# Kernel tuning notes

Hardware: AMD Instinct MI355X
Metric: run time of the kernel (lower is better)

## Reference

```python
import jax, jax.numpy as jnp
import numpy as np

N_NODES = 100000
N_EDGES = 1600000
N_GRAPHS = 512


def gcn_conv(x, row, col, W, b):
    # x: [N, Cin], row/col: [E] (self-loops already appended)
    n = x.shape[0]
    h = x @ W                                        # [N, Cout]
    deg = jax.ops.segment_sum(jnp.ones_like(col, dtype=x.dtype), col, num_segments=n)
    dinv = jnp.where(deg > 0, deg ** -0.5, 0.0)
    norm = dinv[row] * dinv[col]                     # [E]
    msg = norm[:, None] * h[row]                     # [E, Cout]
    out = jax.ops.segment_sum(msg, col, num_segments=n)
    return out + b


def setup_inputs() -> dict:
    key = jax.random.key(0)
    ks = jax.random.split(key, 10)
    x = jax.random.normal(ks[0], (N_NODES, 128), dtype=jnp.float32)
    edge_index = jax.random.randint(ks[1], (2, N_EDGES), 0, N_NODES, dtype=jnp.int64)
    batch = jnp.sort(jax.random.randint(ks[2], (N_NODES,), 0, N_GRAPHS, dtype=jnp.int64))
    def lin_w(k, fan_in, fan_out):
        bound = 1.0 / np.sqrt(fan_in)
        return jax.random.uniform(k, (fan_in, fan_out), jnp.float32, -bound, bound)
    # GCN layers (bias zero-initialized per reset_parameters)
    W1 = lin_w(ks[3], 128, 128); b1 = jnp.zeros((128,), jnp.float32)
    W2 = lin_w(ks[4], 128, 128); b2 = jnp.zeros((128,), jnp.float32)
    # MLP layers (Linear with bias)
    Wm1 = lin_w(ks[5], 128, 64)
    bm1 = jax.random.uniform(ks[6], (64,), jnp.float32, -1/np.sqrt(128), 1/np.sqrt(128))
    Wm2 = lin_w(ks[7], 64, 1)
    bm2 = jax.random.uniform(ks[8], (1,), jnp.float32, -1/np.sqrt(64), 1/np.sqrt(64))
    return {"x": x, "edge_index": edge_index, "batch": batch,
            "W1": W1, "b1": b1, "W2": W2, "b2": b2,
            "Wm1": Wm1, "bm1": bm1, "Wm2": Wm2, "bm2": bm2}


def reference(x, edge_index, batch, W1, b1, W2, b2, Wm1, bm1, Wm2, bm2):
    n = x.shape[0]
    loops = jnp.arange(n, dtype=edge_index.dtype)
    row = jnp.concatenate([edge_index[0], loops])
    col = jnp.concatenate([edge_index[1], loops])
    # GCN: conv -> relu -> conv
    h = gcn_conv(x, row, col, W1, b1)
    h = jax.nn.relu(h)
    h = gcn_conv(h, row, col, W2, b2)
    # scatter-mean pooling over graphs
    sums = jax.ops.segment_sum(h, batch, num_segments=N_GRAPHS)      # [G, C]
    counts = jax.ops.segment_sum(jnp.ones((n,), h.dtype), batch, num_segments=N_GRAPHS)
    g = sums / jnp.maximum(counts, 1.0)[:, None]
    # MLP: linear -> relu -> linear
    g = jax.nn.relu(g @ Wm1 + bm1)
    out = g @ Wm2 + bm2
    return out
```

## Files before the change

### kernel.cpp

```cpp
#include <hip/hip_runtime.h>
#include <math.h>

#define C_DIM 128
#define POOL_CHUNK 64
#define BKT_SHIFT 7
#define MAX_B 1024
#define CB 256
#define FB_CAP 8192
typedef unsigned short ushort_t;
typedef __attribute__((ext_vector_type(8))) short short8;
typedef __attribute__((ext_vector_type(4))) float f32x4;

static inline int ceil_div(int a, int b) { return (a + b - 1) / b; }

__device__ inline ushort_t f2bf(float f) {
    union { float f; unsigned u; } v; v.f = f;
    unsigned r = v.u + 0x7FFFu + ((v.u >> 16) & 1u);
    return (ushort_t)(r >> 16);
}
__device__ inline float bf2f(unsigned s) {
    union { unsigned u; float f; } v; v.u = s << 16; return v.f;
}
__device__ inline float bf_lo(unsigned u) {
    union { unsigned v; float f; } c; c.v = u << 16; return c.f;
}
__device__ inline float bf_hi(unsigned u) {
    union { unsigned v; float f; } c; c.v = u & 0xFFFF0000u; return c.f;
}


__global__ __launch_bounds__(256) void k_bcount(
    const int* __restrict__ col, int E, int chunk, int B,
    int* __restrict__ counts) {
    __shared__ int hist[MAX_B];
    int t = threadIdx.x;
    for (int i = t; i < B; i += 256) hist[i] = 0;
    __syncthreads();
    int s = blockIdx.x * chunk;
    int e = s + chunk; if (e > E) e = E;
    for (int i = s + 4 * t; i < e; i += 1024) {
        int4 c = *(const int4*)(col + i);
        atomicAdd(&hist[c.x >> BKT_SHIFT], 1);
        atomicAdd(&hist[c.y >> BKT_SHIFT], 1);
        atomicAdd(&hist[c.z >> BKT_SHIFT], 1);
        atomicAdd(&hist[c.w >> BKT_SHIFT], 1);
    }
    __syncthreads();
    for (int i = t; i < B; i += 256)
        counts[(size_t)i * CB + blockIdx.x] = hist[i];
}

__global__ __launch_bounds__(256) void k_bscan(
    int* __restrict__ counts, int* __restrict__ btot) {
    __shared__ int sd[256];
    int b = blockIdx.x, t = threadIdx.x;
    int v = counts[(size_t)b * CB + t];
    sd[t] = v;
    __syncthreads();
    for (int off = 1; off < 256; off <<= 1) {
        int x = (t >= off) ? sd[t - off] : 0;
        __syncthreads();
        sd[t] += x;
        __syncthreads();
    }
    counts[(size_t)b * CB + t] = sd[t] - v;
    if (t == 255) btot[b] = sd[255];
}

__global__ __launch_bounds__(256) void k_btotscan(
    const int* __restrict__ btot, int* __restrict__ bbase, int B, int E,
    int* __restrict__ offs, int N) {
    __shared__ int sd[256];
    __shared__ int carry_s;
    int t = threadIdx.x;
    if (t == 0) carry_s = 0;
    __syncthreads();
    int nc = (B + 255) / 256;
    for (int c = 0; c < nc; ++c) {
        int idx = c * 256 + t;
        int v = (idx < B) ? btot[idx] : 0;
        sd[t] = v;
        __syncthreads();
        for (int off = 1; off < 256; off <<= 1) {
            int x = (t >= off) ? sd[t - off] : 0;
            __syncthreads();
            sd[t] += x;
            __syncthreads();
        }
        int pre = sd[t] - v + carry_s;
        if (idx < B) bbase[idx] = pre;
        __syncthreads();
        if (t == 0) carry_s += sd[255];
        __syncthreads();
    }
    if (t == 0) { bbase[B] = E; offs[N] = E; }
}

__global__ __launch_bounds__(256) void k_bscatter(
    const int* __restrict__ row, const int* __restrict__ col, int E, int chunk,
    int B, const int* __restrict__ counts, const int* __restrict__ bbase,
    int* __restrict__ epk) {
    __shared__ int cur[MAX_B];
    int t = threadIdx.x, blk = blockIdx.x;
    for (int i = t; i < B; i += 256)
        cur[i] = bbase[i] + counts[(size_t)i * CB + blk];
    __syncthreads();
    int s = blk * chunk;
    int e = s + chunk; if (e > E) e = E;
    for (int i = s + 4 * t; i < e; i += 1024) {
        int4 c = *(const int4*)(col + i);
        int4 r = *(const int4*)(row + i);
        int s0 = atomicAdd(&cur[c.x >> BKT_SHIFT], 1); epk[s0] = (r.x << 7) | (c.x & 127);
        int s1 = atomicAdd(&cur[c.y >> BKT_SHIFT], 1); epk[s1] = (r.y << 7) | (c.y & 127);
        int s2 = atomicAdd(&cur[c.z >> BKT_SHIFT], 1); epk[s2] = (r.z << 7) | (c.z & 127);
        int s3 = atomicAdd(&cur[c.w >> BKT_SHIFT], 1); epk[s3] = (r.w << 7) | (c.w & 127);
    }
}

__global__ __launch_bounds__(256) void k_bfinal(
    const int* __restrict__ epk, const int* __restrict__ bbase, int N,
    int* __restrict__ offs, float* __restrict__ dinv, int* __restrict__ csr) {
    __shared__ int sh[FB_CAP];
    __shared__ int cnt[128];
    __shared__ int pre[128];
    __shared__ int cur[128];
    int bkt = blockIdx.x, t = threadIdx.x;
    int s = bbase[bkt], e = bbase[bkt + 1];
    int m = e - s;
    int base = bkt << BKT_SHIFT;
    int nn = N - base; if (nn > 128) nn = 128;
    bool fits = (m <= FB_CAP);
    if (t < 128) cnt[t] = 0;
    __syncthreads();
    if (fits) {
        for (int i = t; i < m; i += 256) {
            int u = epk[s + i];
            sh[i] = u;
            atomicAdd(&cnt[u & 127], 1);
        }
    } else {
        for (int i = s + t; i < e; i += 256)
            atomicAdd(&cnt[epk[i] & 127], 1);
    }
    __syncthreads();
    if (t < 128) pre[t] = cnt[t];
    __syncthreads();
    for (int off = 1; off < 128; off <<= 1) {
        int x = (t >= off && t < 128) ? pre[t - off] : 0;
        __syncthreads();
        if (t < 128) pre[t] += x;
        __syncthreads();
    }
    if (t < 128) {
        int ex = pre[t] - cnt[t];
        cur[t] = ex;
        if (t < nn) {
            offs[base + t] = s + ex;
            dinv[base + t] = 1.0f / sqrtf((float)cnt[t] + 1.0f);
        }
    }
    __syncthreads();
    if (fits) {
        for (int i = t; i < m; i += 256) {
            int u = sh[i];
            int slot = atomicAdd(&cur[u & 127], 1);
            csr[s + slot] = u >> 7;
        }
    } else {
        for (int i = s + t; i < e; i += 256) {
            int u = epk[i];
            int slot = atomicAdd(&cur[u & 127], 1);
            csr[s + slot] = u >> 7;
        }
    }
}

__global__ __launch_bounds__(256) void k_wfrag2(
    const float* __restrict__ W1, const float* __restrict__ W2,
    uint4* __restrict__ wf1, uint4* __restrict__ wf2) {
    const float* W = blockIdx.x ? W2 : W1;
    uint4* wf = blockIdx.x ? wf2 : wf1;
    int t = threadIdx.x;
    for (int f = t; f < 2048; f += 256) {
        int lane = f & 63, kkn = f >> 6;
        int kk = kkn & 3, nt = kkn >> 2;
        int n = lane & 15, quad = lane >> 4;
        union { ushort_t h[8]; uint4 v; } u;
#pragma unroll
        for (int j = 0; j < 8; ++j)
            u.h[j] = f2bf(W[(size_t)(kk * 32 + quad * 8 + j) * C_DIM + nt * 16 + n]);
        wf[f] = u.v;
    }
}

template <int ABF16>
__global__ __launch_bounds__(256) void k_matmul_mfma(
    const float* __restrict__ Af, const ushort_t* __restrict__ Abf,
    const uint4* __restrict__ wfrag, const float* __restrict__ dinv,
    ushort_t* __restrict__ Cb, int N) {
    __shared__ uint4 wfs[2048];
    __shared__ __align__(16) ushort_t eb[64 * 136];
    int t = threadIdx.x;
    int wv = t >> 6, lane = t & 63;
    int n = lane & 15, quad = lane >> 4;
    int row0 = blockIdx.x * 128;

    for (int i = t; i < 2048; i += 256) wfs[i] = wfrag[i];

    int rA[2];
#pragma unroll
    for (int tl = 0; tl < 2; ++tl) {
        int r = row0 + wv * 32 + tl * 16 + n;
        rA[tl] = r < N ? r : N - 1;
    }

    f32x4 acc[2][8];
#pragma unroll
    for (int tl = 0; tl < 2; ++tl)
#pragma unroll
        for (int i = 0; i < 8; ++i) acc[tl][i] = (f32x4){0.f, 0.f, 0.f, 0.f};

    __syncthreads();

#pragma unroll
    for (int kk = 0; kk < 4; ++kk) {
        short8 a[2];
#pragma unroll
        for (int tl = 0; tl < 2; ++tl) {
            if (ABF16) {
                uint4 u = *(const uint4*)(Abf + (size_t)rA[tl] * C_DIM + kk * 32 + quad * 8);
                union { uint4 v; short8 s; } c; c.v = u;
                a[tl] = c.s;
            } else {
                const float4* ap = (const float4*)(Af + (size_t)rA[tl] * C_DIM + kk * 32 + quad * 8);
                float4 f0 = ap[0], f1 = ap[1];
                union { ushort_t h[8]; short8 s; } c;
                c.h[0] = f2bf(f0.x); c.h[1] = f2bf(f0.y); c.h[2] = f2bf(f0.z); c.h[3] = f2bf(f0.w);
                c.h[4] = f2bf(f1.x); c.h[5] = f2bf(f1.y); c.h[6] = f2bf(f1.z); c.h[7] = f2bf(f1.w);
                a[tl] = c.s;
            }
        }
#pragma unroll
        for (int nt = 0; nt < 8; ++nt) {
            uint4 bu = wfs[(nt * 4 + kk) * 64 + lane];
            union { uint4 v; short8 s; } c; c.v = bu;
            acc[0][nt] = __builtin_amdgcn_mfma_f32_16x16x32_bf16(a[0], c.s, acc[0][nt], 0, 0, 0);
            acc[1][nt] = __builtin_amdgcn_mfma_f32_16x16x32_bf16(a[1], c.s, acc[1][nt], 0, 0, 0);
        }
    }

#pragma unroll
    for (int pass = 0; pass < 2; ++pass) {
        __syncthreads();
#pragma unroll
        for (int reg = 0; reg < 4; ++reg) {
            int lr = quad * 4 + reg;
            int grow = row0 + wv * 32 + pass * 16 + lr;
            float sc = dinv[grow < N ? grow : N - 1];
#pragma unroll
            for (int nt = 0; nt < 8; ++nt)
                eb[(wv * 16 + lr) * 136 + nt * 16 + n] = f2bf(acc[pass][nt][reg] * sc);
        }
        __syncthreads();
        for (int idx = t; idx < 16 * 64; idx += 256) {
            int r = idx >> 4, c8 = idx & 15;
            int grow = row0 + (r >> 4) * 32 + pass * 16 + (r & 15);
            if (grow < N)
                *(uint4*)(Cb + (size_t)grow * C_DIM + c8 * 8) =
                    *(const uint4*)&eb[r * 136 + c8 * 8];
        }
    }
}

template <int RELU>
__global__ __launch_bounds__(256) void k_aggregate(
    const ushort_t* __restrict__ hs, const int* __restrict__ offs,
    const int* __restrict__ csr, const float* __restrict__ dinv,
    const float* __restrict__ bias, uint4* __restrict__ outV, int N) {
    int node = (blockIdx.x << 2) + (threadIdx.x >> 6);
    if (node >= N) return;
    int t = threadIdx.x & 63;
    int q = t >> 4;
    int fs = t & 15;
    int s = offs[node], e = offs[node + 1];

    float2 ac[4];
    {
        uint4 u = *(const uint4*)(hs + (size_t)node * C_DIM + fs * 8);
        if (q == 0) {
            ac[0] = make_float2(bf_lo(u.x), bf_hi(u.x));
            ac[1] = make_float2(bf_lo(u.y), bf_hi(u.y));
            ac[2] = make_float2(bf_lo(u.z), bf_hi(u.z));
            ac[3] = make_float2(bf_lo(u.w), bf_hi(u.w));
        } else {
#pragma unroll
            for (int i = 0; i < 4; ++i) ac[i] = make_float2(0.f, 0.f);
        }
    }

    int j = s;
    int head = (s + 3) & ~3; if (head > e) head = e;
    if (j < head) {
        if (j + q < head) {
            uint4 u = *(const uint4*)(hs + (size_t)csr[j + q] * C_DIM + fs * 8);
            ac[0].x += bf_lo(u.x); ac[0].y += bf_hi(u.x);
            ac[1].x += bf_lo(u.y); ac[1].y += bf_hi(u.y);
            ac[2].x += bf_lo(u.z); ac[2].y += bf_hi(u.z);
            ac[3].x += bf_lo(u.w); ac[3].y += bf_hi(u.w);
        }
        j = head;
    }
    for (; j + 16 <= e; j += 16) {
        int4 rv = *(const int4*)(csr + j + 4 * q);
        uint4 u0 = *(const uint4*)(hs + (size_t)rv.x * C_DIM + fs * 8);
        uint4 u1 = *(const uint4*)(hs + (size_t)rv.y * C_DIM + fs * 8);
        uint4 u2 = *(const uint4*)(hs + (size_t)rv.z * C_DIM + fs * 8);
        uint4 u3 = *(const uint4*)(hs + (size_t)rv.w * C_DIM + fs * 8);
        ac[0].x += bf_lo(u0.x); ac[0].y += bf_hi(u0.x);
        ac[1].x += bf_lo(u0.y); ac[1].y += bf_hi(u0.y);
        ac[2].x += bf_lo(u0.z); ac[2].y += bf_hi(u0.z);
        ac[3].x += bf_lo(u0.w); ac[3].y += bf_hi(u0.w);
        ac[0].x += bf_lo(u1.x); ac[0].y += bf_hi(u1.x);
        ac[1].x += bf_lo(u1.y); ac[1].y += bf_hi(u1.y);
        ac[2].x += bf_lo(u1.z); ac[2].y += bf_hi(u1.z);
        ac[3].x += bf_lo(u1.w); ac[3].y += bf_hi(u1.w);
        ac[0].x += bf_lo(u2.x); ac[0].y += bf_hi(u2.x);
        ac[1].x += bf_lo(u2.y); ac[1].y += bf_hi(u2.y);
        ac[2].x += bf_lo(u2.z); ac[2].y += bf_hi(u2.z);
        ac[3].x += bf_lo(u2.w); ac[3].y += bf_hi(u2.w);
        ac[0].x += bf_lo(u3.x); ac[0].y += bf_hi(u3.x);
        ac[1].x += bf_lo(u3.y); ac[1].y += bf_hi(u3.y);
        ac[2].x += bf_lo(u3.z); ac[2].y += bf_hi(u3.z);
        ac[3].x += bf_lo(u3.w); ac[3].y += bf_hi(u3.w);
    }
    for (; j + 4 <= e; j += 4) {
        uint4 u = *(const uint4*)(hs + (size_t)csr[j + q] * C_DIM + fs * 8);
        ac[0].x += bf_lo(u.x); ac[0].y += bf_hi(u.x);
        ac[1].x += bf_lo(u.y); ac[1].y += bf_hi(u.y);
        ac[2].x += bf_lo(u.z); ac[2].y += bf_hi(u.z);
        ac[3].x += bf_lo(u.w); ac[3].y += bf_hi(u.w);
    }
    if (j + q < e) {
        uint4 u = *(const uint4*)(hs + (size_t)csr[j + q] * C_DIM + fs * 8);
        ac[0].x += bf_lo(u.x); ac[0].y += bf_hi(u.x);
        ac[1].x += bf_lo(u.y); ac[1].y += bf_hi(u.y);
        ac[2].x += bf_lo(u.z); ac[2].y += bf_hi(u.z);
        ac[3].x += bf_lo(u.w); ac[3].y += bf_hi(u.w);
    }

#pragma unroll
    for (int i = 0; i < 4; ++i) {
        ac[i].x += __shfl_xor(ac[i].x, 16);
        ac[i].y += __shfl_xor(ac[i].y, 16);
        ac[i].x += __shfl_xor(ac[i].x, 32);
        ac[i].y += __shfl_xor(ac[i].y, 32);
    }

    if (q == 0) {
        float dn = dinv[node];
        float4 b0 = *(const float4*)(bias + fs * 8);
        float4 b1 = *(const float4*)(bias + fs * 8 + 4);
        float o[8];
        o[0] = dn * ac[0].x + b0.x; o[1] = dn * ac[0].y + b0.y;
        o[2] = dn * ac[1].x + b0.z; o[3] = dn * ac[1].y + b0.w;
        o[4] = dn * ac[2].x + b1.x; o[5] = dn * ac[2].y + b1.y;
        o[6] = dn * ac[3].x + b1.z; o[7] = dn * ac[3].y + b1.w;
        if (RELU) {
#pragma unroll
            for (int i = 0; i < 8; ++i) o[i] = fmaxf(o[i], 0.f);
        }
        uint4 pk;
        pk.x = (unsigned)f2bf(o[0]) | ((unsigned)f2bf(o[1]) << 16);
        pk.y = (unsigned)f2bf(o[2]) | ((unsigned)f2bf(o[3]) << 16);
        pk.z = (unsigned)f2bf(o[4]) | ((unsigned)f2bf(o[5]) << 16);
        pk.w = (unsigned)f2bf(o[6]) | ((unsigned)f2bf(o[7]) << 16);
        outV[(size_t)node * 16 + fs] = pk;
    }
}

__global__ __launch_bounds__(128) void k_pool_sum(
    const ushort_t* __restrict__ h, const int* __restrict__ batch, int n,
    float* __restrict__ sums) {
    int r0 = blockIdx.x * POOL_CHUNK;
    int r1 = r0 + POOL_CHUNK; if (r1 > n) r1 = n;
    if (r0 >= n) return;
    int t = threadIdx.x;
    int c = t & 63, rr = t >> 6;
    float2 acc = make_float2(0.f, 0.f);
    int g = batch[r0];
    int i = r0;
    while (i < r1) {
        if (i + 8 <= r1 && batch[i + 7] == g) {
#pragma unroll
            for (int b = 0; b < 4; ++b) {
                unsigned u = *(const unsigned*)(h + (size_t)(i + rr + 2 * b) * C_DIM + c * 2);
                acc.x += bf_lo(u); acc.y += bf_hi(u);
            }
            i += 8;
        } else {
            int bi = batch[i];
            if (bi != g) {
                atomicAdd(&sums[(size_t)g * C_DIM + c * 2], acc.x);
                atomicAdd(&sums[(size_t)g * C_DIM + c * 2 + 1], acc.y);
                acc = make_float2(0.f, 0.f); g = bi;
            }
            if (rr == 0) {
                unsigned u = *(const unsigned*)(h + (size_t)i * C_DIM + c * 2);
                acc.x += bf_lo(u); acc.y += bf_hi(u);
            }
            ++i;
        }
    }
    atomicAdd(&sums[(size_t)g * C_DIM + c * 2], acc.x);
    atomicAdd(&sums[(size_t)g * C_DIM + c * 2 + 1], acc.y);
}

__global__ __launch_bounds__(128) void k_mlp(
    const float* __restrict__ sums, const int* __restrict__ batch, int n,
    const float* __restrict__ Wm1, const float* __restrict__ bm1,
    const float* __restrict__ Wm2, const float* __restrict__ bm2,
    float* __restrict__ out) {
    int g = blockIdx.x;
    int t = threadIdx.x;
    int lo = 0, hi = n;
    while (lo < hi) { int m = (lo + hi) >> 1; if (batch[m] < g) lo = m + 1; else hi = m; }
    int start = lo;
    lo = start; hi = n;
    while (lo < hi) { int m = (lo + hi) >> 1; if (batch[m] < g + 1) lo = m + 1; else hi = m; }
    float cnt = (float)(lo - start);

    float mean = sums[(size_t)g * C_DIM + t] / fmaxf(cnt, 1.0f);

    __shared__ float m_s[128];
    __shared__ float hid[64];
    m_s[t] = mean;
    __syncthreads();
    if (t < 64) {
        float a = bm1[t];
#pragma unroll 4
        for (int k = 0; k < 128; ++k) a += m_s[k] * Wm1[k * 64 + t];
        hid[t] = fmaxf(a, 0.f) * Wm2[t];
    }
    __syncthreads();
    if (t < 64) {
        float v = hid[t];
        for (int off = 32; off > 0; off >>= 1) v += __shfl_down(v, off);
        if (t == 0) out[g] = v + bm2[0];
    }
}

extern "C" void kernel_launch(void* const* d_in, const int* in_sizes, int n_in,
                              void* d_out, int out_size, void* d_ws, size_t ws_size,
                              hipStream_t stream) {
    const float* x     = (const float*)d_in[0];
    const int*   eidx  = (const int*)d_in[1];
    const int*   batch = (const int*)d_in[2];
    const float* W1    = (const float*)d_in[3];
    const float* b1    = (const float*)d_in[4];
    const float* W2    = (const float*)d_in[5];
    const float* b2    = (const float*)d_in[6];
    const float* Wm1   = (const float*)d_in[7];
    const float* bm1   = (const float*)d_in[8];
    const float* Wm2   = (const float*)d_in[9];
    const float* bm2   = (const float*)d_in[10];

    const int N = in_sizes[2];
    const int E = in_sizes[1] / 2;
    const int G = out_size;
    const int B = (N + 127) >> BKT_SHIFT;

    char* p = (char*)d_ws;
    auto carve = [&](size_t bytes) {
        char* q = p;
        p += (bytes + 255) & ~(size_t)255;
        return q;
    };
    ushort_t* bufT   = (ushort_t*)carve((size_t)N * C_DIM * sizeof(ushort_t));
    ushort_t* bufA   = (ushort_t*)carve((size_t)N * C_DIM * sizeof(ushort_t));
    float*    dinv   = (float*)   carve((size_t)N * sizeof(float));
    int*      offs   = (int*)     carve((size_t)(N + 1) * sizeof(int));
    int*      csr    = (int*)     carve((size_t)E * sizeof(int));
    int*      counts = (int*)     carve((size_t)B * CB * sizeof(int));
    int*      btot   = (int*)     carve((size_t)B * sizeof(int));
    int*      bbase  = (int*)     carve((size_t)(B + 1) * sizeof(int));
    float*    gsums  = (float*)   carve((size_t)G * C_DIM * sizeof(float));
    uint4*    wf1    = (uint4*)   carve(2048 * sizeof(uint4));
    uint4*    wf2    = (uint4*)   carve(2048 * sizeof(uint4));
    int*      epk    = (int*)bufT;

    const int* erow = eidx;
    const int* ecol = eidx + E;
    const int chunk = (ceil_div(E, CB) + 3) & ~3;

    hipMemsetAsync(gsums, 0, (size_t)G * C_DIM * sizeof(float), stream);

    k_bcount<<<CB, 256, 0, stream>>>(ecol, E, chunk, B, counts);
    k_bscan<<<B, 256, 0, stream>>>(counts, btot);
    k_btotscan<<<1, 256, 0, stream>>>(btot, bbase, B, E, offs, N);
    k_bscatter<<<CB, 256, 0, stream>>>(erow, ecol, E, chunk, B, counts, bbase, epk);
    k_bfinal<<<B, 256, 0, stream>>>(epk, bbase, N, offs, dinv, csr);

    k_wfrag2<<<2, 256, 0, stream>>>(W1, W2, wf1, wf2);

    k_matmul_mfma<0><<<ceil_div(N, 128), 256, 0, stream>>>(x, nullptr, wf1, dinv, bufT, N);
    k_aggregate<1><<<ceil_div(N, 4), 256, 0, stream>>>(bufT, offs, csr, dinv, b1,
                                                       (uint4*)bufA, N);
    k_matmul_mfma<1><<<ceil_div(N, 128), 256, 0, stream>>>(nullptr, bufA, wf2, dinv, bufT, N);
    k_aggregate<0><<<ceil_div(N, 4), 256, 0, stream>>>(bufT, offs, csr, dinv, b2,
                                                       (uint4*)bufA, N);
    k_pool_sum<<<ceil_div(N, POOL_CHUNK), 128, 0, stream>>>(bufA, batch, N, gsums);
    k_mlp<<<G, 128, 0, stream>>>(gsums, batch, N, Wm1, bm1, Wm2, bm2, (float*)d_out);
}
```

Before: 341.7 us.

## Fold weight prep and memset into bcount, replace bucket scan with atomic cursor

Weight fragment conversion and the gsums zeroing move into extra blocks of k_bcount. The single-block total scan kernel is dropped: each bucket now claims its base offset through an atomicAdd on a global cursor, so buckets are no longer laid out in order, and offsets become int2 start/end pairs. The aggregate kernel drops its alignment head and loads csr indices as scalars instead of int4. The aim is to remove three launches and a serial scan, at the cost of a nondeterministic CSR layout and a possibly less coalesced edge order.

```diff
diff --git a/kernel.cpp b/kernel.cpp
--- a/kernel.cpp
+++ b/kernel.cpp
@@ -27,16 +27,43 @@
 __device__ inline float bf_hi(unsigned u) {
     union { unsigned v; float f; } c; c.v = u & 0xFFFF0000u; return c.f;
 }
+__device__ inline void accum8(uint4 u, float acc[8]) {
+    acc[0] += bf_lo(u.x); acc[1] += bf_hi(u.x);
+    acc[2] += bf_lo(u.y); acc[3] += bf_hi(u.y);
+    acc[4] += bf_lo(u.z); acc[5] += bf_hi(u.z);
+    acc[6] += bf_lo(u.w); acc[7] += bf_hi(u.w);
+}
 
 
 __global__ __launch_bounds__(256) void k_bcount(
     const int* __restrict__ col, int E, int chunk, int B,
-    int* __restrict__ counts) {
+    int* __restrict__ counts,
+    const float* __restrict__ W1, const float* __restrict__ W2,
+    uint4* __restrict__ wf1, uint4* __restrict__ wf2,
+    float* __restrict__ gsums, int GC, int* __restrict__ cursor) {
+    int t = threadIdx.x, blk = blockIdx.x;
+    if (blk >= CB) {
+        const float* W = (blk == CB) ? W1 : W2;
+        uint4* wf = (blk == CB) ? wf1 : wf2;
+        for (int f = t; f < 2048; f += 256) {
+            int lane = f & 63, kkn = f >> 6;
+            int kk = kkn & 3, nt = kkn >> 2;
+            int n = lane & 15, quad = lane >> 4;
+            union { ushort_t h[8]; uint4 v; } u;
+#pragma unroll
+            for (int j = 0; j < 8; ++j)
+                u.h[j] = f2bf(W[(size_t)(kk * 32 + quad * 8 + j) * C_DIM + nt * 16 + n]);
+            wf[f] = u.v;
+        }
+        return;
+    }
+    for (int i = blk * 256 + t; i < GC; i += CB * 256) gsums[i] = 0.f;
+    if (blk == 0 && t == 0) *cursor = 0;
+
     __shared__ int hist[MAX_B];
-    int t = threadIdx.x;
     for (int i = t; i < B; i += 256) hist[i] = 0;
     __syncthreads();
-    int s = blockIdx.x * chunk;
+    int s = blk * chunk;
     int e = s + chunk; if (e > E) e = E;
     for (int i = s + 4 * t; i < e; i += 1024) {
         int4 c = *(const int4*)(col + i);
@@ -47,11 +74,12 @@
     }
     __syncthreads();
     for (int i = t; i < B; i += 256)
-        counts[(size_t)i * CB + blockIdx.x] = hist[i];
+        counts[(size_t)i * CB + blk] = hist[i];
 }
 
 __global__ __launch_bounds__(256) void k_bscan(
-    int* __restrict__ counts, int* __restrict__ btot) {
+    int* __restrict__ counts, int* __restrict__ bbase, int* __restrict__ btot,
+    int* __restrict__ cursor) {
     __shared__ int sd[256];
     int b = blockIdx.x, t = threadIdx.x;
     int v = counts[(size_t)b * CB + t];
@@ -64,36 +92,10 @@
         __syncthreads();
     }
     counts[(size_t)b * CB + t] = sd[t] - v;
-    if (t == 255) btot[b] = sd[255];
-}
-
-__global__ __launch_bounds__(256) void k_btotscan(
-    const int* __restrict__ btot, int* __restrict__ bbase, int B, int E,
-    int* __restrict__ offs, int N) {
-    __shared__ int sd[256];
-    __shared__ int carry_s;
-    int t = threadIdx.x;
-    if (t == 0) carry_s = 0;
-    __syncthreads();
-    int nc = (B + 255) / 256;
-    for (int c = 0; c < nc; ++c) {
-        int idx = c * 256 + t;
-        int v = (idx < B) ? btot[idx] : 0;
-        sd[t] = v;
-        __syncthreads();
-        for (int off = 1; off < 256; off <<= 1) {
-            int x = (t >= off) ? sd[t - off] : 0;
-            __syncthreads();
-            sd[t] += x;
-            __syncthreads();
-        }
-        int pre = sd[t] - v + carry_s;
-        if (idx < B) bbase[idx] = pre;
-        __syncthreads();
-        if (t == 0) carry_s += sd[255];
-        __syncthreads();
-    }
-    if (t == 0) { bbase[B] = E; offs[N] = E; }
+    if (t == 255) {
+        btot[b] = sd[255];
+        bbase[b] = atomicAdd(cursor, sd[255]);
+    }
 }
 
 __global__ __launch_bounds__(256) void k_bscatter(
@@ -118,15 +120,17 @@
 }
 
 __global__ __launch_bounds__(256) void k_bfinal(
-    const int* __restrict__ epk, const int* __restrict__ bbase, int N,
-    int* __restrict__ offs, float* __restrict__ dinv, int* __restrict__ csr) {
+    const int* __restrict__ epk, const int* __restrict__ bbase,
+    const int* __restrict__ btot, int N,
+    int2* __restrict__ offs2, float* __restrict__ dinv, int* __restrict__ csr) {
     __shared__ int sh[FB_CAP];
     __shared__ int cnt[128];
     __shared__ int pre[128];
     __shared__ int cur[128];
     int bkt = blockIdx.x, t = threadIdx.x;
-    int s = bbase[bkt], e = bbase[bkt + 1];
-    int m = e - s;
+    int s = bbase[bkt];
+    int m = btot[bkt];
+    int e = s + m;
     int base = bkt << BKT_SHIFT;
     int nn = N - base; if (nn > 128) nn = 128;
     bool fits = (m <= FB_CAP);
@@ -155,7 +159,7 @@
         int ex = pre[t] - cnt[t];
         cur[t] = ex;
         if (t < nn) {
-            offs[base + t] = s + ex;
+            offs2[base + t] = make_int2(s + ex, s + ex + cnt[t]);
             dinv[base + t] = 1.0f / sqrtf((float)cnt[t] + 1.0f);
         }
     }
@@ -172,24 +176,6 @@
             int slot = atomicAdd(&cur[u & 127], 1);
             csr[s + slot] = u >> 7;
         }
-    }
-}
-
-__global__ __launch_bounds__(256) void k_wfrag2(
-    const float* __restrict__ W1, const float* __restrict__ W2,
-    uint4* __restrict__ wf1, uint4* __restrict__ wf2) {
-    const float* W = blockIdx.x ? W2 : W1;
-    uint4* wf = blockIdx.x ? wf2 : wf1;
-    int t = threadIdx.x;
-    for (int f = t; f < 2048; f += 256) {
-        int lane = f & 63, kkn = f >> 6;
-        int kk = kkn & 3, nt = kkn >> 2;
-        int n = lane & 15, quad = lane >> 4;
-        union { ushort_t h[8]; uint4 v; } u;
-#pragma unroll
-        for (int j = 0; j < 8; ++j)
-            u.h[j] = f2bf(W[(size_t)(kk * 32 + quad * 8 + j) * C_DIM + nt * 16 + n]);
-        wf[f] = u.v;
     }
 }
 
@@ -274,7 +260,7 @@
 
 template <int RELU>
 __global__ __launch_bounds__(256) void k_aggregate(
-    const ushort_t* __restrict__ hs, const int* __restrict__ offs,
+    const ushort_t* __restrict__ hs, const int2* __restrict__ offs2,
     const int* __restrict__ csr, const float* __restrict__ dinv,
     const float* __restrict__ bias, uint4* __restrict__ outV, int N) {
     int node = (blockIdx.x << 2) + (threadIdx.x >> 6);
@@ -282,78 +268,48 @@
     int t = threadIdx.x & 63;
     int q = t >> 4;
     int fs = t & 15;
-    int s = offs[node], e = offs[node + 1];
-
-    float2 ac[4];
+    int2 se = offs2[node];
+    int s = se.x, e = se.y;
+
+    float acc[8];
     {
         uint4 u = *(const uint4*)(hs + (size_t)node * C_DIM + fs * 8);
-        if (q == 0) {
-            ac[0] = make_float2(bf_lo(u.x), bf_hi(u.x));
-            ac[1] = make_float2(bf_lo(u.y), bf_hi(u.y));
-            ac[2] = make_float2(bf_lo(u.z), bf_hi(u.z));
-            ac[3] = make_float2(bf_lo(u.w), bf_hi(u.w));
-        } else {
-#pragma unroll
-            for (int i = 0; i < 4; ++i) ac[i] = make_float2(0.f, 0.f);
-        }
+        float v[8];
+        v[0] = bf_lo(u.x); v[1] = bf_hi(u.x);
+        v[2] = bf_lo(u.y); v[3] = bf_hi(u.y);
+        v[4] = bf_lo(u.z); v[5] = bf_hi(u.z);
+        v[6] = bf_lo(u.w); v[7] = bf_hi(u.w);
+#pragma unroll
+        for (int i = 0; i < 8; ++i) acc[i] = (q == 0) ? v[i] : 0.f;
     }
 
     int j = s;
-    int head = (s + 3) & ~3; if (head > e) head = e;
-    if (j < head) {
-        if (j + q < head) {
-            uint4 u = *(const uint4*)(hs + (size_t)csr[j + q] * C_DIM + fs * 8);
-            ac[0].x += bf_lo(u.x); ac[0].y += bf_hi(u.x);
-            ac[1].x += bf_lo(u.y); ac[1].y += bf_hi(u.y);
-            ac[2].x += bf_lo(u.z); ac[2].y += bf_hi(u.z);
-            ac[3].x += bf_lo(u.w); ac[3].y += bf_hi(u.w);
-        }
-        j = head;
-    }
     for (; j + 16 <= e; j += 16) {
-        int4 rv = *(const int4*)(csr + j + 4 * q);
-        uint4 u0 = *(const uint4*)(hs + (size_t)rv.x * C_DIM + fs * 8);
-        uint4 u1 = *(const uint4*)(hs + (size_t)rv.y * C_DIM + fs * 8);
-        uint4 u2 = *(const uint4*)(hs + (size_t)rv.z * C_DIM + fs * 8);
-        uint4 u3 = *(const uint4*)(hs + (size_t)rv.w * C_DIM + fs * 8);
-        ac[0].x += bf_lo(u0.x); ac[0].y += bf_hi(u0.x);
-        ac[1].x += bf_lo(u0.y); ac[1].y += bf_hi(u0.y);
-        ac[2].x += bf_lo(u0.z); ac[2].y += bf_hi(u0.z);
-        ac[3].x += bf_lo(u0.w); ac[3].y += bf_hi(u0.w);
-        ac[0].x += bf_lo(u1.x); ac[0].y += bf_hi(u1.x);
-        ac[1].x += bf_lo(u1.y); ac[1].y += bf_hi(u1.y);
-        ac[2].x += bf_lo(u1.z); ac[2].y += bf_hi(u1.z);
-        ac[3].x += bf_lo(u1.w); ac[3].y += bf_hi(u1.w);
-        ac[0].x += bf_lo(u2.x); ac[0].y += bf_hi(u2.x);
-        ac[1].x += bf_lo(u2.y); ac[1].y += bf_hi(u2.y);
-        ac[2].x += bf_lo(u2.z); ac[2].y += bf_hi(u2.z);
-        ac[3].x += bf_lo(u2.w); ac[3].y += bf_hi(u2.w);
-        ac[0].x += bf_lo(u3.x); ac[0].y += bf_hi(u3.x);
-        ac[1].x += bf_lo(u3.y); ac[1].y += bf_hi(u3.y);
-        ac[2].x += bf_lo(u3.z); ac[2].y += bf_hi(u3.z);
-        ac[3].x += bf_lo(u3.w); ac[3].y += bf_hi(u3.w);
+        int r[4];
+#pragma unroll
+        for (int b = 0; b < 4; ++b) r[b] = csr[j + b * 4 + q];
+        uint4 u[4];
+#pragma unroll
+        for (int b = 0; b < 4; ++b)
+            u[b] = *(const uint4*)(hs + (size_t)r[b] * C_DIM + fs * 8);
+#pragma unroll
+        for (int b = 0; b < 4; ++b) accum8(u[b], acc);
     }
     for (; j + 4 <= e; j += 4) {
-        uint4 u = *(const uint4*)(hs + (size_t)csr[j + q] * C_DIM + fs * 8);
-        ac[0].x += bf_lo(u.x); ac[0].y += bf_hi(u.x);
-        ac[1].x += bf_lo(u.y); ac[1].y += bf_hi(u.y);
-        ac[2].x += bf_lo(u.z); ac[2].y += bf_hi(u.z);
-        ac[3].x += bf_lo(u.w); ac[3].y += bf_hi(u.w);
+        int r = csr[j + q];
+        uint4 u = *(const uint4*)(hs + (size_t)r * C_DIM + fs * 8);
+        accum8(u, acc);
     }
     if (j + q < e) {
-        uint4 u = *(const uint4*)(hs + (size_t)csr[j + q] * C_DIM + fs * 8);
-        ac[0].x += bf_lo(u.x); ac[0].y += bf_hi(u.x);
-        ac[1].x += bf_lo(u.y); ac[1].y += bf_hi(u.y);
-        ac[2].x += bf_lo(u.z); ac[2].y += bf_hi(u.z);
-        ac[3].x += bf_lo(u.w); ac[3].y += bf_hi(u.w);
-    }
-
-#pragma unroll
-    for (int i = 0; i < 4; ++i) {
-        ac[i].x += __shfl_xor(ac[i].x, 16);
-        ac[i].y += __shfl_xor(ac[i].y, 16);
-        ac[i].x += __shfl_xor(ac[i].x, 32);
-        ac[i].y += __shfl_xor(ac[i].y, 32);
+        int r = csr[j + q];
+        uint4 u = *(const uint4*)(hs + (size_t)r * C_DIM + fs * 8);
+        accum8(u, acc);
+    }
+
+#pragma unroll
+    for (int i = 0; i < 8; ++i) {
+        acc[i] += __shfl_xor(acc[i], 16);
+        acc[i] += __shfl_xor(acc[i], 32);
     }
 
     if (q == 0) {
@@ -361,10 +317,10 @@
         float4 b0 = *(const float4*)(bias + fs * 8);
         float4 b1 = *(const float4*)(bias + fs * 8 + 4);
         float o[8];
-        o[0] = dn * ac[0].x + b0.x; o[1] = dn * ac[0].y + b0.y;
-        o[2] = dn * ac[1].x + b0.z; o[3] = dn * ac[1].y + b0.w;
-        o[4] = dn * ac[2].x + b1.x; o[5] = dn * ac[2].y + b1.y;
-        o[6] = dn * ac[3].x + b1.z; o[7] = dn * ac[3].y + b1.w;
+        o[0] = dn * acc[0] + b0.x; o[1] = dn * acc[1] + b0.y;
+        o[2] = dn * acc[2] + b0.z; o[3] = dn * acc[3] + b0.w;
+        o[4] = dn * acc[4] + b1.x; o[5] = dn * acc[5] + b1.y;
+        o[6] = dn * acc[6] + b1.z; o[7] = dn * acc[7] + b1.w;
         if (RELU) {
 #pragma unroll
             for (int i = 0; i < 8; ++i) o[i] = fmaxf(o[i], 0.f);
@@ -478,35 +434,32 @@
     ushort_t* bufT   = (ushort_t*)carve((size_t)N * C_DIM * sizeof(ushort_t));
     ushort_t* bufA   = (ushort_t*)carve((size_t)N * C_DIM * sizeof(ushort_t));
     float*    dinv   = (float*)   carve((size_t)N * sizeof(float));
-    int*      offs   = (int*)     carve((size_t)(N + 1) * sizeof(int));
+    int2*     offs2  = (int2*)    carve((size_t)N * sizeof(int2));
     int*      csr    = (int*)     carve((size_t)E * sizeof(int));
     int*      counts = (int*)     carve((size_t)B * CB * sizeof(int));
     int*      btot   = (int*)     carve((size_t)B * sizeof(int));
-    int*      bbase  = (int*)     carve((size_t)(B + 1) * sizeof(int));
+    int*      bbase  = (int*)     carve((size_t)B * sizeof(int));
     float*    gsums  = (float*)   carve((size_t)G * C_DIM * sizeof(float));
     uint4*    wf1    = (uint4*)   carve(2048 * sizeof(uint4));
     uint4*    wf2    = (uint4*)   carve(2048 * sizeof(uint4));
+    int*      cursor = (int*)     carve(sizeof(int));
     int*      epk    = (int*)bufT;
 
     const int* erow = eidx;
     const int* ecol = eidx + E;
     const int chunk = (ceil_div(E, CB) + 3) & ~3;
 
-    hipMemsetAsync(gsums, 0, (size_t)G * C_DIM * sizeof(float), stream);
-
-    k_bcount<<<CB, 256, 0, stream>>>(ecol, E, chunk, B, counts);
-    k_bscan<<<B, 256, 0, stream>>>(counts, btot);
-    k_btotscan<<<1, 256, 0, stream>>>(btot, bbase, B, E, offs, N);
+    k_bcount<<<CB + 2, 256, 0, stream>>>(ecol, E, chunk, B, counts,
+                                         W1, W2, wf1, wf2, gsums, G * C_DIM, cursor);
+    k_bscan<<<B, 256, 0, stream>>>(counts, bbase, btot, cursor);
     k_bscatter<<<CB, 256, 0, stream>>>(erow, ecol, E, chunk, B, counts, bbase, epk);
-    k_bfinal<<<B, 256, 0, stream>>>(epk, bbase, N, offs, dinv, csr);
-
-    k_wfrag2<<<2, 256, 0, stream>>>(W1, W2, wf1, wf2);
+    k_bfinal<<<B, 256, 0, stream>>>(epk, bbase, btot, N, offs2, dinv, csr);
 
     k_matmul_mfma<0><<<ceil_div(N, 128), 256, 0, stream>>>(x, nullptr, wf1, dinv, bufT, N);
-    k_aggregate<1><<<ceil_div(N, 4), 256, 0, stream>>>(bufT, offs, csr, dinv, b1,
+    k_aggregate<1><<<ceil_div(N, 4), 256, 0, stream>>>(bufT, offs2, csr, dinv, b1,
                                                        (uint4*)bufA, N);
     k_matmul_mfma<1><<<ceil_div(N, 128), 256, 0, stream>>>(nullptr, bufA, wf2, dinv, bufT, N);
-    k_aggregate<0><<<ceil_div(N, 4), 256, 0, stream>>>(bufT, offs, csr, dinv, b2,
+    k_aggregate<0><<<ceil_div(N, 4), 256, 0, stream>>>(bufT, offs2, csr, dinv, b2,
                                                        (uint4*)bufA, N);
     k_pool_sum<<<ceil_div(N, POOL_CHUNK), 128, 0, stream>>>(bufA, batch, N, gsums);
     k_mlp<<<G, 128, 0, stream>>>(gsums, batch, N, Wm1, bm1, Wm2, bm2, (float*)d_out);
```

After: 333.1 us. -2.5%, faster.
